# Kernel tuning notes

Hardware: AMD Instinct MI355X
Metric: run time of the kernel (lower is better)

Reference implementation:

```python
import jax, jax.numpy as jnp
import numpy as np

N_NODES = 100000
N_EDGES = 1600000
D_FEAT = 64


def setup_inputs() -> dict:
    key = jax.random.key(0)
    k1, k2 = jax.random.split(key)
    x = jax.random.normal(k1, (N_NODES, D_FEAT), dtype=jnp.float32)
    edge_index = jax.random.randint(k2, (2, N_EDGES), 0, N_NODES, dtype=jnp.int64)
    return {"x": x, "edge_index": edge_index}


def reference(x, edge_index):
    # LightGCN propagation: out = D^{-1/2} A D^{-1/2} x with A given in COO form.
    row, col = edge_index[0], edge_index[1]
    n = x.shape[0]
    # deg[i] = number of edges with row == i (torch.sparse.sum over dim=1 of ones)
    deg = jax.ops.segment_sum(jnp.ones_like(row, dtype=x.dtype), row, num_segments=n)
    deg_inv_sqrt = jnp.where(deg > 0, jax.lax.rsqrt(jnp.maximum(deg, 1.0)), 0.0)
    norm = deg_inv_sqrt[row] * deg_inv_sqrt[col]  # [E]
    # SpMM: out[row] += norm * x[col]  (gather-scale-scatter-reduce)
    messages = norm[:, None] * x[col]  # [E, d]
    out = jax.ops.segment_sum(messages, row, num_segments=n)  # [N, d]
    return out
```

## Files before the change

### kernel.cpp

```cpp
#include <hip/hip_runtime.h>
#include <hip/hip_fp16.h>

#define N_NODES 100000
#define D_FEAT 64
#define RPB 256
#define NB ((N_NODES + RPB - 1) / RPB)
#define CAP 6144
#define CHUNK 4096
#define COL_BITS 17
#define COL_MASK ((1 << COL_BITS) - 1)

typedef float vfloat4 __attribute__((ext_vector_type(4)));

__global__ void zero_kernel(int* __restrict__ p, int n) {
    int i = blockIdx.x * blockDim.x + threadIdx.x;
    if (i < n) p[i] = 0;
}

__global__ void __launch_bounds__(256)
part_kernel(const int* __restrict__ row, const int* __restrict__ col,
            int* __restrict__ bucketCursor,
            int* __restrict__ packed, int E) {
    __shared__ int h[NB];
    __shared__ int rbase[NB];
    __shared__ int ebuf[CHUNK];
    __shared__ unsigned short bkbuf[CHUNK];
    int t = threadIdx.x;
    for (int i = t; i < NB; i += 256) h[i] = 0;
    __syncthreads();
    int lo = blockIdx.x * CHUNK;
    int cnt = min(CHUNK, E - lo);
    for (int i = t; i < cnt; i += 256) {
        int e = lo + i;
        int r = row[e], c = col[e];
        int bk = r >> 8;
        ebuf[i] = ((r & (RPB - 1)) << COL_BITS) | c;
        bkbuf[i] = (unsigned short)bk;
        atomicAdd(&h[bk], 1);
    }
    __syncthreads();
    for (int i = t; i < NB; i += 256) {
        int c2 = h[i];
        rbase[i] = c2 ? atomicAdd(&bucketCursor[i], c2) : 0;
        h[i] = 0;
    }
    __syncthreads();
    for (int i = t; i < cnt; i += 256) {
        int bk = bkbuf[i];
        int pos = rbase[bk] + atomicAdd(&h[bk], 1);
        if (pos < CAP)
            packed[bk * CAP + pos] = ebuf[i];
    }
}

__global__ void __launch_bounds__(256)
csr_build_kernel(int* __restrict__ packed,
                 const int* __restrict__ bucketCursor,
                 int4* __restrict__ rowSED,
                 const float* __restrict__ x, __half* __restrict__ xs, int N) {
    __shared__ int ebuf[CAP];
    __shared__ int cnt[RPB];
    __shared__ int scn[RPB];
    __shared__ int cur[RPB];
    __shared__ float disS[RPB];
    int b = blockIdx.x, t = threadIdx.x;
    int base = b * CAP;
    int n = min(bucketCursor[b], CAP);
    for (int i = t; i < n; i += 256) ebuf[i] = packed[base + i];
    cnt[t] = 0;
    __syncthreads();
    for (int i = t; i < n; i += 256)
        atomicAdd(&cnt[ebuf[i] >> COL_BITS], 1);
    __syncthreads();
    int v = cnt[t];
    scn[t] = v;
    __syncthreads();
    for (int o = 1; o < RPB; o <<= 1) {
        int u = (t >= o) ? scn[t - o] : 0;
        __syncthreads();
        scn[t] += u;
        __syncthreads();
    }
    int ex = scn[t] - v;
    cur[t] = ex;
    float d = (v > 0) ? rsqrtf((float)v) : 0.0f;
    disS[t] = d;
    int r = b * RPB + t;
    if (r < N)
        rowSED[r] = make_int4(base + ex, base + ex + v, __float_as_int(d), 0);
    __syncthreads();
    for (int i = t; i < n; i += 256) {
        int p = ebuf[i];
        int lr = p >> COL_BITS;
        int pos = base + atomicAdd(&cur[lr], 1);
        packed[pos] = p & COL_MASK;
    }
    long long rowBase = (long long)b * RPB;
    #pragma unroll 4
    for (int i = t; i < RPB * (D_FEAT / 4); i += 256) {
        int lr = i >> 4;
        long long rr = rowBase + lr;
        if (rr < N) {
            const vfloat4* xp = (const vfloat4*)(x + (rr << 6) + ((i & 15) << 2));
            vfloat4 vv = __builtin_nontemporal_load(xp);
            float dd = disS[lr];
            __half2 h0 = __floats2half2_rn(dd * vv.x, dd * vv.y);
            __half2 h1 = __floats2half2_rn(dd * vv.z, dd * vv.w);
            uint2 u;
            u.x = *(unsigned int*)&h0;
            u.y = *(unsigned int*)&h1;
            *(uint2*)(xs + (rr << 6) + ((i & 15) << 2)) = u;
        }
    }
}

__device__ __forceinline__ void addp(__half2* a, uint4 v) {
    __half2* hp = (__half2*)&v;
    a[0] = __hadd2(a[0], hp[0]);
    a[1] = __hadd2(a[1], hp[1]);
    a[2] = __hadd2(a[2], hp[2]);
    a[3] = __hadd2(a[3], hp[3]);
}
__device__ __forceinline__ void fmap(__half2* a, uint4 v, __half2 w2) {
    __half2* hp = (__half2*)&v;
    a[0] = __hfma2(hp[0], w2, a[0]);
    a[1] = __hfma2(hp[1], w2, a[1]);
    a[2] = __hfma2(hp[2], w2, a[2]);
    a[3] = __hfma2(hp[3], w2, a[3]);
}

__global__ void __launch_bounds__(1024)
spmm_h8_kernel(const __half* __restrict__ xs,
               const int4* __restrict__ rowSED,
               const int* __restrict__ csr_col,
               float* __restrict__ out, int N) {
    int wid = blockIdx.x * 16 + (threadIdx.x >> 6);
    if (wid >= N) return;
    int lane = threadIdx.x & 63;
    int g = lane >> 3;
    int q = lane & 7;
    int4 sed = rowSED[wid];
    int s = sed.x, e = sed.y;
    float dr = __int_as_float(sed.z);
    __half2 acc[4];
    acc[0] = __float2half2_rn(0.f);
    acc[1] = acc[0]; acc[2] = acc[0]; acc[3] = acc[0];
    int j = s;
    for (; j + 32 <= e; j += 32) {
        int c0 = __builtin_nontemporal_load(&csr_col[j + g]);
        int c1 = __builtin_nontemporal_load(&csr_col[j + 8 + g]);
        int c2 = __builtin_nontemporal_load(&csr_col[j + 16 + g]);
        int c3 = __builtin_nontemporal_load(&csr_col[j + 24 + g]);
        uint4 v0 = *(const uint4*)(xs + (c0 << 6) + (q << 3));
        uint4 v1 = *(const uint4*)(xs + (c1 << 6) + (q << 3));
        uint4 v2 = *(const uint4*)(xs + (c2 << 6) + (q << 3));
        uint4 v3 = *(const uint4*)(xs + (c3 << 6) + (q << 3));
        addp(acc, v0); addp(acc, v1); addp(acc, v2); addp(acc, v3);
    }
    {
        int last = e - 1;
        int n0 = j + g, n1 = n0 + 8, n2 = n0 + 16, n3 = n0 + 24;
        int i0 = max(min(n0, last), 0);
        int i1 = max(min(n1, last), 0);
        int i2 = max(min(n2, last), 0);
        int i3 = max(min(n3, last), 0);
        int c0 = __builtin_nontemporal_load(&csr_col[i0]) & COL_MASK;
        int c1 = __builtin_nontemporal_load(&csr_col[i1]) & COL_MASK;
        int c2 = __builtin_nontemporal_load(&csr_col[i2]) & COL_MASK;
        int c3 = __builtin_nontemporal_load(&csr_col[i3]) & COL_MASK;
        uint4 v0 = *(const uint4*)(xs + (c0 << 6) + (q << 3));
        uint4 v1 = *(const uint4*)(xs + (c1 << 6) + (q << 3));
        uint4 v2 = *(const uint4*)(xs + (c2 << 6) + (q << 3));
        uint4 v3 = *(const uint4*)(xs + (c3 << 6) + (q << 3));
        __half2 w0 = __float2half2_rn((n0 < e) ? 1.0f : 0.0f);
        __half2 w1 = __float2half2_rn((n1 < e) ? 1.0f : 0.0f);
        __half2 w2 = __float2half2_rn((n2 < e) ? 1.0f : 0.0f);
        __half2 w3 = __float2half2_rn((n3 < e) ? 1.0f : 0.0f);
        fmap(acc, v0, w0); fmap(acc, v1, w1); fmap(acc, v2, w2); fmap(acc, v3, w3);
    }
    #pragma unroll
    for (int k = 0; k < 4; ++k) {
        int a = *(int*)&acc[k];
        int b8 = __shfl_xor(a, 8);
        acc[k] = __hadd2(acc[k], *(__half2*)&b8);
        a = *(int*)&acc[k];
        int b16 = __shfl_xor(a, 16);
        acc[k] = __hadd2(acc[k], *(__half2*)&b16);
        a = *(int*)&acc[k];
        int b32 = __shfl_xor(a, 32);
        acc[k] = __hadd2(acc[k], *(__half2*)&b32);
    }
    if (g == 0) {
        float2 f0 = __half22float2(acc[0]);
        float2 f1 = __half22float2(acc[1]);
        float2 f2 = __half22float2(acc[2]);
        float2 f3 = __half22float2(acc[3]);
        vfloat4 o0, o1;
        o0.x = dr * f0.x; o0.y = dr * f0.y; o0.z = dr * f1.x; o0.w = dr * f1.y;
        o1.x = dr * f2.x; o1.y = dr * f2.y; o1.z = dr * f3.x; o1.w = dr * f3.y;
        float* op = out + ((long long)wid << 6) + (q << 3);
        __builtin_nontemporal_store(o0, (vfloat4*)op);
        __builtin_nontemporal_store(o1, (vfloat4*)(op + 4));
    }
}

__global__ void fb_deg_kernel(const int* __restrict__ row, float* __restrict__ deg, int E) {
    int i = blockIdx.x * blockDim.x + threadIdx.x;
    int stride = gridDim.x * blockDim.x;
    for (; i < E; i += stride) atomicAdd(&deg[row[i]], 1.0f);
}
__global__ void fb_dis_kernel(float* __restrict__ deg, int N) {
    int i = blockIdx.x * blockDim.x + threadIdx.x;
    if (i < N) { float d = deg[i]; deg[i] = (d > 0.0f) ? rsqrtf(d) : 0.0f; }
}
__global__ void fb_scatter_kernel(const float* __restrict__ x, const int* __restrict__ row,
                                  const int* __restrict__ col, const float* __restrict__ dis,
                                  float* __restrict__ out, long long total) {
    long long i = (long long)blockIdx.x * blockDim.x + threadIdx.x;
    long long stride = (long long)gridDim.x * blockDim.x;
    for (; i < total; i += stride) {
        int e = (int)(i >> 6);
        int d = (int)(i & 63);
        int r = row[e];
        int c = col[e];
        atomicAdd(&out[(long long)r * D_FEAT + d], dis[r] * dis[c] * x[(long long)c * D_FEAT + d]);
    }
}

extern "C" void kernel_launch(void* const* d_in, const int* in_sizes, int n_in,
                              void* d_out, int out_size, void* d_ws, size_t ws_size,
                              hipStream_t stream) {
    const float* x  = (const float*)d_in[0];
    const int*   ei = (const int*)d_in[1];
    int E = in_sizes[1] / 2;
    const int* row = ei;
    const int* col = ei + E;
    float* out = (float*)d_out;
    const int N = N_NODES;

    size_t need = (size_t)NB * CAP * 4 + (size_t)N * D_FEAT * 2
                + (size_t)N * 16 + (size_t)NB * 4;

    if (ws_size >= need) {
        char* ws = (char*)d_ws;
        int*    packed       = (int*)ws;    ws += (size_t)NB * CAP * 4;
        __half* xs           = (__half*)ws; ws += (size_t)N * D_FEAT * 2;
        int4*   rowSED       = (int4*)ws;   ws += (size_t)N * 16;
        int*    bucketCursor = (int*)ws;

        zero_kernel<<<1, 512, 0, stream>>>(bucketCursor, NB);
        int nChunks = (E + CHUNK - 1) / CHUNK;
        part_kernel<<<nChunks, 256, 0, stream>>>(row, col, bucketCursor, packed, E);
        csr_build_kernel<<<NB, RPB, 0, stream>>>(packed, bucketCursor, rowSED, x, xs, N);
        spmm_h8_kernel<<<(N + 15) / 16, 1024, 0, stream>>>(xs, rowSED, packed, out, N);
        return;
    }

    float* deg = (float*)d_ws;
    (void)hipMemsetAsync(out, 0, (size_t)out_size * sizeof(float), stream);
    (void)hipMemsetAsync(deg, 0, (size_t)N * sizeof(float), stream);
    fb_deg_kernel<<<2048, 256, 0, stream>>>(row, deg, E);
    fb_dis_kernel<<<(N + 255) / 256, 256, 0, stream>>>(deg, N);
    fb_scatter_kernel<<<4096, 256, 0, stream>>>(x, row, col, deg, out, (long long)E * D_FEAT);
}
```

Measured before the change: 92.41 us.

## Drop LDS staging in partition kernel and stage CSR scatter through shared memory

The partition kernel stops buffering packed edges in shared memory and instead reads row/col from global memory twice, which frees LDS and may allow more blocks per CU. The CSR build kernel now scatters column indices into a shared buffer and then writes them back to global memory coalesced, replacing random global writes. It also launches 512 threads per block instead of 256, with the scan and per-row work guarded to the first 256 threads. The costs are a second global read of the edge arrays and roughly twice the LDS per CSR block, which may lower occupancy there.

```diff
diff --git a/kernel.cpp b/kernel.cpp
--- a/kernel.cpp
+++ b/kernel.cpp
@@ -23,21 +23,13 @@
             int* __restrict__ packed, int E) {
     __shared__ int h[NB];
     __shared__ int rbase[NB];
-    __shared__ int ebuf[CHUNK];
-    __shared__ unsigned short bkbuf[CHUNK];
     int t = threadIdx.x;
     for (int i = t; i < NB; i += 256) h[i] = 0;
     __syncthreads();
     int lo = blockIdx.x * CHUNK;
-    int cnt = min(CHUNK, E - lo);
-    for (int i = t; i < cnt; i += 256) {
-        int e = lo + i;
-        int r = row[e], c = col[e];
-        int bk = r >> 8;
-        ebuf[i] = ((r & (RPB - 1)) << COL_BITS) | c;
-        bkbuf[i] = (unsigned short)bk;
-        atomicAdd(&h[bk], 1);
-    }
+    int hi = min(lo + CHUNK, E);
+    for (int e = lo + t; e < hi; e += 256)
+        atomicAdd(&h[row[e] >> 8], 1);
     __syncthreads();
     for (int i = t; i < NB; i += 256) {
         int c2 = h[i];
@@ -45,20 +37,22 @@
         h[i] = 0;
     }
     __syncthreads();
-    for (int i = t; i < cnt; i += 256) {
-        int bk = bkbuf[i];
+    for (int e = lo + t; e < hi; e += 256) {
+        int r = row[e], c = col[e];
+        int bk = r >> 8;
         int pos = rbase[bk] + atomicAdd(&h[bk], 1);
         if (pos < CAP)
-            packed[bk * CAP + pos] = ebuf[i];
-    }
-}
-
-__global__ void __launch_bounds__(256)
+            packed[bk * CAP + pos] = ((r & (RPB - 1)) << COL_BITS) | c;
+    }
+}
+
+__global__ void __launch_bounds__(512)
 csr_build_kernel(int* __restrict__ packed,
                  const int* __restrict__ bucketCursor,
                  int4* __restrict__ rowSED,
                  const float* __restrict__ x, __half* __restrict__ xs, int N) {
     __shared__ int ebuf[CAP];
+    __shared__ int sbuf[CAP];
     __shared__ int cnt[RPB];
     __shared__ int scn[RPB];
     __shared__ int cur[RPB];
@@ -66,38 +60,43 @@
     int b = blockIdx.x, t = threadIdx.x;
     int base = b * CAP;
     int n = min(bucketCursor[b], CAP);
-    for (int i = t; i < n; i += 256) ebuf[i] = packed[base + i];
-    cnt[t] = 0;
-    __syncthreads();
-    for (int i = t; i < n; i += 256)
+    for (int i = t; i < n; i += 512) ebuf[i] = packed[base + i];
+    if (t < RPB) cnt[t] = 0;
+    __syncthreads();
+    for (int i = t; i < n; i += 512)
         atomicAdd(&cnt[ebuf[i] >> COL_BITS], 1);
     __syncthreads();
-    int v = cnt[t];
-    scn[t] = v;
+    int v = 0;
+    if (t < RPB) { v = cnt[t]; scn[t] = v; }
     __syncthreads();
     for (int o = 1; o < RPB; o <<= 1) {
-        int u = (t >= o) ? scn[t - o] : 0;
+        int u = 0;
+        if (t < RPB && t >= o) u = scn[t - o];
         __syncthreads();
-        scn[t] += u;
+        if (t < RPB) scn[t] += u;
         __syncthreads();
     }
-    int ex = scn[t] - v;
-    cur[t] = ex;
-    float d = (v > 0) ? rsqrtf((float)v) : 0.0f;
-    disS[t] = d;
-    int r = b * RPB + t;
-    if (r < N)
-        rowSED[r] = make_int4(base + ex, base + ex + v, __float_as_int(d), 0);
-    __syncthreads();
-    for (int i = t; i < n; i += 256) {
+    if (t < RPB) {
+        int ex = scn[t] - v;
+        cur[t] = ex;
+        float d = (v > 0) ? rsqrtf((float)v) : 0.0f;
+        disS[t] = d;
+        int r = b * RPB + t;
+        if (r < N)
+            rowSED[r] = make_int4(base + ex, base + ex + v, __float_as_int(d), 0);
+    }
+    __syncthreads();
+    for (int i = t; i < n; i += 512) {
         int p = ebuf[i];
         int lr = p >> COL_BITS;
-        int pos = base + atomicAdd(&cur[lr], 1);
-        packed[pos] = p & COL_MASK;
-    }
+        int pos = atomicAdd(&cur[lr], 1);
+        sbuf[pos] = p & COL_MASK;
+    }
+    __syncthreads();
+    for (int i = t; i < n; i += 512)
+        packed[base + i] = sbuf[i];
     long long rowBase = (long long)b * RPB;
-    #pragma unroll 4
-    for (int i = t; i < RPB * (D_FEAT / 4); i += 256) {
+    for (int i = t; i < RPB * (D_FEAT / 4); i += 512) {
         int lr = i >> 4;
         long long rr = rowBase + lr;
         if (rr < N) {
@@ -251,7 +250,7 @@
         zero_kernel<<<1, 512, 0, stream>>>(bucketCursor, NB);
         int nChunks = (E + CHUNK - 1) / CHUNK;
         part_kernel<<<nChunks, 256, 0, stream>>>(row, col, bucketCursor, packed, E);
-        csr_build_kernel<<<NB, RPB, 0, stream>>>(packed, bucketCursor, rowSED, x, xs, N);
+        csr_build_kernel<<<NB, 512, 0, stream>>>(packed, bucketCursor, rowSED, x, xs, N);
         spmm_h8_kernel<<<(N + 15) / 16, 1024, 0, stream>>>(xs, rowSED, packed, out, N);
         return;
     }
```

Measured after the change: 86.70 us. -6.2%, faster.
